# Performance work log

Measured on AMD Instinct MI355X. Metric: run time of the kernel, lower is better.

## Reference

```python
import jax, jax.numpy as jnp
import numpy as np

B, L, C, R = 4, 2048, 16, 16
A_SCALE = 0.05  # keep spectral radius of transition matrices < 1 over L=2048 steps


def setup_inputs() -> dict:
    key = jax.random.key(0)
    k1, k2 = jax.random.split(key)
    A = jax.random.normal(k1, (B, L, C, R, R), dtype=jnp.float32) * A_SCALE
    X = jax.random.normal(k2, (B, L, C, R, R), dtype=jnp.float32)
    return {"A": A, "X": X}


def reference(A, X):
    # Linear matrix recurrence: Y_t = A_t @ Y_{t-1} + X_t (Y_0 = X_0),
    # computed in log-depth via an associative scan over the time axis (L).
    # Combine rule matches the Triton scan_combine_matrix:
    #   a_new = a_curr @ a_prev;  x_new = a_curr @ x_prev + x_curr
    def combine(e1, e2):
        a1, x1 = e1  # earlier segment
        a2, x2 = e2  # later segment
        a = jnp.einsum('blcik,blckj->blcij', a2, a1)
        x = jnp.einsum('blcik,blckj->blcij', a2, x1) + x2
        return (a, x)

    _, Y = jax.lax.associative_scan(combine, (A, X), axis=1)
    return Y  # [B, L, C, R, R]
```

## Files before the change

kernel.cpp:

```cpp
#include <hip/hip_runtime.h>

constexpr int B = 4, L = 2048, C = 16, R = 16;
constexpr int M = R * R;
constexpr int G = 64;
constexpr int S = L / G;
constexpr int T = 4;

__device__ __forceinline__ long mat_off(int b, int l, int c) {
    return (((long)b * L + l) * C + c) * M;
}

__global__ __launch_bounds__(256) void pass1_chunk_agg(
    const float* __restrict__ A, const float* __restrict__ X,
    float* __restrict__ ws) {
    const int blk = blockIdx.x;
    const int g   = blk % G;
    const int bc  = blk / G;
    const int b   = bc / C, c = bc % C;
    const int tid = threadIdx.x;
    const int i = tid >> 4, j = tid & 15;

    __shared__ float sA[T][M];
    __shared__ float sX[T][M];
    __shared__ float aggA[M];
    __shared__ float aggX[M];

    aggA[tid] = (i == j) ? 1.0f : 0.0f;
    aggX[tid] = 0.0f;

    const int tm = tid >> 6;
    const int e4 = (tid & 63) << 2;

    for (int t0 = 0; t0 < S; t0 += T) {
        const int l = g * S + t0 + tm;
        const float4 va = *(const float4*)(A + mat_off(b, l, c) + e4);
        const float4 vx = *(const float4*)(X + mat_off(b, l, c) + e4);
        *(float4*)&sA[tm][e4] = va;
        *(float4*)&sX[tm][e4] = vx;
        __syncthreads();
        for (int s = 0; s < T; ++s) {
            float accA = 0.0f;
            float accX = sX[s][tid];
            #pragma unroll
            for (int k = 0; k < 16; ++k) {
                const float a = sA[s][(i << 4) + k];
                accA += a * aggA[(k << 4) + j];
                accX += a * aggX[(k << 4) + j];
            }
            __syncthreads();
            aggA[tid] = accA;
            aggX[tid] = accX;
            __syncthreads();
        }
    }
    float* slot = ws + (long)blk * (2 * M);
    slot[tid]     = aggA[tid];
    slot[M + tid] = aggX[tid];
}

__global__ __launch_bounds__(256) void pass2_scan(float* __restrict__ ws) {
    const int bc  = blockIdx.x;
    const int tid = threadIdx.x;
    const int i = tid >> 4, j = tid & 15;

    __shared__ float sAg[M];
    __shared__ float carry[M];
    carry[tid] = 0.0f;

    float* base = ws + (long)bc * G * (2 * M);
    for (int g = 0; g < G; ++g) {
        float* slot = base + (long)g * (2 * M);
        sAg[tid] = slot[tid];
        const float xg  = slot[M + tid];
        const float old = carry[tid];
        __syncthreads();
        float acc = xg;
        #pragma unroll
        for (int k = 0; k < 16; ++k)
            acc += sAg[(i << 4) + k] * carry[(k << 4) + j];
        slot[M + tid] = old;
        __syncthreads();
        carry[tid] = acc;
        __syncthreads();
    }
}

__global__ __launch_bounds__(256) void pass3_apply(
    const float* __restrict__ A, const float* __restrict__ X,
    const float* __restrict__ ws, float* __restrict__ out) {
    const int blk = blockIdx.x;
    const int g   = blk % G;
    const int bc  = blk / G;
    const int b   = bc / C, c = bc % C;
    const int tid = threadIdx.x;
    const int i = tid >> 4, j = tid & 15;

    __shared__ float sA[T][M];
    __shared__ float sX[T][M];
    __shared__ float Y[M];

    Y[tid] = ws[(long)blk * (2 * M) + M + tid];

    const int tm = tid >> 6;
    const int e4 = (tid & 63) << 2;

    for (int t0 = 0; t0 < S; t0 += T) {
        const int l = g * S + t0 + tm;
        const float4 va = *(const float4*)(A + mat_off(b, l, c) + e4);
        const float4 vx = *(const float4*)(X + mat_off(b, l, c) + e4);
        *(float4*)&sA[tm][e4] = va;
        *(float4*)&sX[tm][e4] = vx;
        __syncthreads();
        for (int s = 0; s < T; ++s) {
            float acc = sX[s][tid];
            #pragma unroll
            for (int k = 0; k < 16; ++k)
                acc += sA[s][(i << 4) + k] * Y[(k << 4) + j];
            __syncthreads();
            Y[tid] = acc;
            out[mat_off(b, g * S + t0 + s, c) + tid] = acc;
            __syncthreads();
        }
    }
}

extern "C" void kernel_launch(void* const* d_in, const int* in_sizes, int n_in,
                              void* d_out, int out_size, void* d_ws, size_t ws_size,
                              hipStream_t stream) {
    const float* A = (const float*)d_in[0];
    const float* X = (const float*)d_in[1];
    float* out = (float*)d_out;
    float* ws  = (float*)d_ws;

    pass1_chunk_agg<<<B * C * G, 256, 0, stream>>>(A, X, ws);
    pass2_scan<<<B * C, 256, 0, stream>>>(ws);
    pass3_apply<<<B * C * G, 256, 0, stream>>>(A, X, ws, out);
}
```

Before: 401.3 us.

## Use split-bf16 MFMA per wavefront for chunk aggregation and apply passes

```diff
diff --git a/kernel.cpp b/kernel.cpp
--- a/kernel.cpp
+++ b/kernel.cpp
@@ -4,58 +4,128 @@
 constexpr int M = R * R;
 constexpr int G = 64;
 constexpr int S = L / G;
-constexpr int T = 4;
+constexpr int LSTRIDE = C * M;
+
+typedef __attribute__((ext_vector_type(4))) float        f32x4;
+typedef __attribute__((ext_vector_type(8))) short        bf16x8;
+typedef __attribute__((ext_vector_type(4))) unsigned int u32x4;
 
 __device__ __forceinline__ long mat_off(int b, int l, int c) {
     return (((long)b * L + l) * C + c) * M;
 }
 
-__global__ __launch_bounds__(256) void pass1_chunk_agg(
-    const float* __restrict__ A, const float* __restrict__ X,
-    float* __restrict__ ws) {
-    const int blk = blockIdx.x;
-    const int g   = blk % G;
-    const int bc  = blk / G;
-    const int b   = bc / C, c = bc % C;
-    const int tid = threadIdx.x;
-    const int i = tid >> 4, j = tid & 15;
-
-    __shared__ float sA[T][M];
-    __shared__ float sX[T][M];
-    __shared__ float aggA[M];
-    __shared__ float aggX[M];
-
-    aggA[tid] = (i == j) ? 1.0f : 0.0f;
-    aggX[tid] = 0.0f;
-
-    const int tm = tid >> 6;
-    const int e4 = (tid & 63) << 2;
-
-    for (int t0 = 0; t0 < S; t0 += T) {
-        const int l = g * S + t0 + tm;
-        const float4 va = *(const float4*)(A + mat_off(b, l, c) + e4);
-        const float4 vx = *(const float4*)(X + mat_off(b, l, c) + e4);
-        *(float4*)&sA[tm][e4] = va;
-        *(float4*)&sX[tm][e4] = vx;
-        __syncthreads();
-        for (int s = 0; s < T; ++s) {
-            float accA = 0.0f;
-            float accX = sX[s][tid];
+__device__ __forceinline__ unsigned pack_hi16(float lo, float hi) {
+    return (__float_as_uint(lo) >> 16) | (__float_as_uint(hi) & 0xFFFF0000u);
+}
+__device__ __forceinline__ float trunc_bf(float v) {
+    return __uint_as_float(__float_as_uint(v) & 0xFFFF0000u);
+}
+__device__ __forceinline__ bf16x8 frag_from(unsigned d0, unsigned d1,
+                                            unsigned d2, unsigned d3) {
+    u32x4 u = {d0, d1, d2, d3};
+    return __builtin_bit_cast(bf16x8, u);
+}
+
+__device__ __forceinline__ bf16x8 make_a_frag(const f32x4& lo4, const f32x4& hi4,
+                                              bool lowk) {
+    float a0 = lo4[0], a1 = lo4[1], a2 = lo4[2], a3 = lo4[3];
+    float a4 = hi4[0], a5 = hi4[1], a6 = hi4[2], a7 = hi4[3];
+    unsigned h0 = pack_hi16(a0, a1), h1 = pack_hi16(a2, a3);
+    unsigned h2 = pack_hi16(a4, a5), h3 = pack_hi16(a6, a7);
+    unsigned l0 = pack_hi16(a0 - trunc_bf(a0), a1 - trunc_bf(a1));
+    unsigned l1 = pack_hi16(a2 - trunc_bf(a2), a3 - trunc_bf(a3));
+    unsigned l2 = pack_hi16(a4 - trunc_bf(a4), a5 - trunc_bf(a5));
+    unsigned l3 = pack_hi16(a6 - trunc_bf(a6), a7 - trunc_bf(a7));
+    return lowk ? frag_from(h0, h1, h2, h3) : frag_from(l0, l1, l2, l3);
+}
+
+__device__ __forceinline__ void make_b_frags(const f32x4& y, int s0, int s1,
+                                             bf16x8& bh, bf16x8& bl) {
+    unsigned yh01 = pack_hi16(y[0], y[1]);
+    unsigned yh23 = pack_hi16(y[2], y[3]);
+    unsigned yl01 = pack_hi16(y[0] - trunc_bf(y[0]), y[1] - trunc_bf(y[1]));
+    unsigned yl23 = pack_hi16(y[2] - trunc_bf(y[2]), y[3] - trunc_bf(y[3]));
+    unsigned b0 = (unsigned)__shfl((int)yh01, s0, 64);
+    unsigned b1 = (unsigned)__shfl((int)yh23, s0, 64);
+    unsigned b2 = (unsigned)__shfl((int)yh01, s1, 64);
+    unsigned b3 = (unsigned)__shfl((int)yh23, s1, 64);
+    unsigned c0 = (unsigned)__shfl((int)yl01, s0, 64);
+    unsigned c1 = (unsigned)__shfl((int)yl23, s0, 64);
+    unsigned c2 = (unsigned)__shfl((int)yl01, s1, 64);
+    unsigned c3 = (unsigned)__shfl((int)yl23, s1, 64);
+    bh = frag_from(b0, b1, b2, b3);
+    bl = frag_from(c0, c1, c2, c3);
+}
+
+__global__ __launch_bounds__(256) void pass1_mfma(const float* __restrict__ A,
+                                                  const float* __restrict__ X,
+                                                  float* __restrict__ ws) {
+    const int lane  = threadIdx.x & 63;
+    const int chunk = blockIdx.x * 4 + (threadIdx.x >> 6);
+    const int g  = chunk % G;
+    const int bc = chunk / G;
+    const int b  = bc / C, c = bc % C;
+
+    const int  mn   = lane & 15;
+    const int  kg   = lane >> 4;
+    const bool lowk = kg < 2;
+    const int  kb   = (kg & 1) * 8;
+    const int  s0   = (kg & 1) * 32 + mn;
+    const int  s1   = s0 + 16;
+    const int  arow = mn * 16 + kb;
+
+    const float* Ap = A + mat_off(b, g * S, c);
+    const float* Xp = X + mat_off(b, g * S, c);
+
+    unsigned id[4];
+    #pragma unroll
+    for (int r = 0; r < 4; ++r) {
+        int k0 = kb + 2 * r;
+        unsigned v = 0u;
+        if (k0 == mn)     v |= 0x3F80u;
+        if (k0 + 1 == mn) v |= 0x3F800000u;
+        id[r] = v;
+    }
+    bf16x8 BAh = frag_from(id[0], id[1], id[2], id[3]);
+    bf16x8 BAl = frag_from(0, 0, 0, 0);
+    bf16x8 BXh = frag_from(0, 0, 0, 0);
+    bf16x8 BXl = BXh;
+
+    f32x4 aLo = *(const f32x4*)(Ap + arow);
+    f32x4 aHi = *(const f32x4*)(Ap + arow + 4);
+    f32x4 xc;
+    #pragma unroll
+    for (int r = 0; r < 4; ++r) xc[r] = Xp[(4 * kg + r) * 16 + mn];
+
+    f32x4 accA, accX;
+    const f32x4 zero = {0.f, 0.f, 0.f, 0.f};
+    for (int t = 0; t < S; ++t) {
+        f32x4 aLoN, aHiN, xcN;
+        if (t < S - 1) {
+            const float* An = Ap + (t + 1) * LSTRIDE;
+            const float* Xn = Xp + (t + 1) * LSTRIDE;
+            aLoN = *(const f32x4*)(An + arow);
+            aHiN = *(const f32x4*)(An + arow + 4);
             #pragma unroll
-            for (int k = 0; k < 16; ++k) {
-                const float a = sA[s][(i << 4) + k];
-                accA += a * aggA[(k << 4) + j];
-                accX += a * aggX[(k << 4) + j];
-            }
-            __syncthreads();
-            aggA[tid] = accA;
-            aggX[tid] = accX;
-            __syncthreads();
-        }
-    }
-    float* slot = ws + (long)blk * (2 * M);
-    slot[tid]     = aggA[tid];
-    slot[M + tid] = aggX[tid];
+            for (int r = 0; r < 4; ++r) xcN[r] = Xn[(4 * kg + r) * 16 + mn];
+        }
+        const bf16x8 Af = make_a_frag(aLo, aHi, lowk);
+        accA = __builtin_amdgcn_mfma_f32_16x16x32_bf16(Af, BAh, zero, 0, 0, 0);
+        accA = __builtin_amdgcn_mfma_f32_16x16x32_bf16(Af, BAl, accA, 0, 0, 0);
+        accX = __builtin_amdgcn_mfma_f32_16x16x32_bf16(Af, BXh, xc,   0, 0, 0);
+        accX = __builtin_amdgcn_mfma_f32_16x16x32_bf16(Af, BXl, accX, 0, 0, 0);
+        if (t < S - 1) {
+            make_b_frags(accA, s0, s1, BAh, BAl);
+            make_b_frags(accX, s0, s1, BXh, BXl);
+            aLo = aLoN; aHi = aHiN; xc = xcN;
+        }
+    }
+    float* slot = ws + (long)chunk * (2 * M);
+    #pragma unroll
+    for (int r = 0; r < 4; ++r) {
+        slot[(4 * kg + r) * 16 + mn]     = accA[r];
+        slot[M + (4 * kg + r) * 16 + mn] = accX[r];
+    }
 }
 
 __global__ __launch_bounds__(256) void pass2_scan(float* __restrict__ ws) {
@@ -68,10 +138,17 @@
     carry[tid] = 0.0f;
 
     float* base = ws + (long)bc * G * (2 * M);
+    float curA = base[tid];
+    float curX = base[M + tid];
     for (int g = 0; g < G; ++g) {
         float* slot = base + (long)g * (2 * M);
-        sAg[tid] = slot[tid];
-        const float xg  = slot[M + tid];
+        float nA = 0.f, nX = 0.f;
+        if (g < G - 1) {
+            nA = slot[2 * M + tid];
+            nX = slot[2 * M + M + tid];
+        }
+        sAg[tid] = curA;
+        const float xg  = curX;
         const float old = carry[tid];
         __syncthreads();
         float acc = xg;
@@ -82,44 +159,65 @@
         __syncthreads();
         carry[tid] = acc;
         __syncthreads();
-    }
-}
-
-__global__ __launch_bounds__(256) void pass3_apply(
-    const float* __restrict__ A, const float* __restrict__ X,
-    const float* __restrict__ ws, float* __restrict__ out) {
-    const int blk = blockIdx.x;
-    const int g   = blk % G;
-    const int bc  = blk / G;
-    const int b   = bc / C, c = bc % C;
-    const int tid = threadIdx.x;
-    const int i = tid >> 4, j = tid & 15;
-
-    __shared__ float sA[T][M];
-    __shared__ float sX[T][M];
-    __shared__ float Y[M];
-
-    Y[tid] = ws[(long)blk * (2 * M) + M + tid];
-
-    const int tm = tid >> 6;
-    const int e4 = (tid & 63) << 2;
-
-    for (int t0 = 0; t0 < S; t0 += T) {
-        const int l = g * S + t0 + tm;
-        const float4 va = *(const float4*)(A + mat_off(b, l, c) + e4);
-        const float4 vx = *(const float4*)(X + mat_off(b, l, c) + e4);
-        *(float4*)&sA[tm][e4] = va;
-        *(float4*)&sX[tm][e4] = vx;
-        __syncthreads();
-        for (int s = 0; s < T; ++s) {
-            float acc = sX[s][tid];
+        curA = nA; curX = nX;
+    }
+}
+
+__global__ __launch_bounds__(256) void pass3_mfma(const float* __restrict__ A,
+                                                  const float* __restrict__ X,
+                                                  const float* __restrict__ ws,
+                                                  float* __restrict__ out) {
+    const int lane  = threadIdx.x & 63;
+    const int chunk = blockIdx.x * 4 + (threadIdx.x >> 6);
+    const int g  = chunk % G;
+    const int bc = chunk / G;
+    const int b  = bc / C, c = bc % C;
+
+    const int  mn   = lane & 15;
+    const int  kg   = lane >> 4;
+    const bool lowk = kg < 2;
+    const int  kb   = (kg & 1) * 8;
+    const int  s0   = (kg & 1) * 32 + mn;
+    const int  s1   = s0 + 16;
+    const int  arow = mn * 16 + kb;
+
+    const float* Ap = A + mat_off(b, g * S, c);
+    const float* Xp = X + mat_off(b, g * S, c);
+    float*       Op = out + mat_off(b, g * S, c);
+
+    const float* slot = ws + (long)chunk * (2 * M);
+    f32x4 Y;
+    #pragma unroll
+    for (int r = 0; r < 4; ++r) Y[r] = slot[M + (4 * kg + r) * 16 + mn];
+
+    bf16x8 Bh, Bl;
+    make_b_frags(Y, s0, s1, Bh, Bl);
+
+    f32x4 aLo = *(const f32x4*)(Ap + arow);
+    f32x4 aHi = *(const f32x4*)(Ap + arow + 4);
+    f32x4 xc;
+    #pragma unroll
+    for (int r = 0; r < 4; ++r) xc[r] = Xp[(4 * kg + r) * 16 + mn];
+
+    for (int t = 0; t < S; ++t) {
+        f32x4 aLoN, aHiN, xcN;
+        if (t < S - 1) {
+            const float* An = Ap + (t + 1) * LSTRIDE;
+            const float* Xn = Xp + (t + 1) * LSTRIDE;
+            aLoN = *(const f32x4*)(An + arow);
+            aHiN = *(const f32x4*)(An + arow + 4);
             #pragma unroll
-            for (int k = 0; k < 16; ++k)
-                acc += sA[s][(i << 4) + k] * Y[(k << 4) + j];
-            __syncthreads();
-            Y[tid] = acc;
-            out[mat_off(b, g * S + t0 + s, c) + tid] = acc;
-            __syncthreads();
+            for (int r = 0; r < 4; ++r) xcN[r] = Xn[(4 * kg + r) * 16 + mn];
+        }
+        const bf16x8 Af = make_a_frag(aLo, aHi, lowk);
+        f32x4 acc = __builtin_amdgcn_mfma_f32_16x16x32_bf16(Af, Bh, xc, 0, 0, 0);
+        acc = __builtin_amdgcn_mfma_f32_16x16x32_bf16(Af, Bl, acc, 0, 0, 0);
+        float* o = Op + t * LSTRIDE;
+        #pragma unroll
+        for (int r = 0; r < 4; ++r) o[(4 * kg + r) * 16 + mn] = acc[r];
+        if (t < S - 1) {
+            make_b_frags(acc, s0, s1, Bh, Bl);
+            aLo = aLoN; aHi = aHiN; xc = xcN;
         }
     }
 }
@@ -132,7 +230,7 @@
     float* out = (float*)d_out;
     float* ws  = (float*)d_ws;
 
-    pass1_chunk_agg<<<B * C * G, 256, 0, stream>>>(A, X, ws);
+    pass1_mfma<<<B * C * G / 4, 256, 0, stream>>>(A, X, ws);
     pass2_scan<<<B * C, 256, 0, stream>>>(ws);
-    pass3_apply<<<B * C * G, 256, 0, stream>>>(A, X, ws, out);
-}
+    pass3_mfma<<<B * C * G / 4, 256, 0, stream>>>(A, X, ws, out);
+}
```

Result: faster. 391.4 us (-2.5%).
